# Optimization experiments

Hardware: AMD Instinct MI355X
Metric: run time of the kernel (lower is better)

## Reference

```python
import jax, jax.numpy as jnp
import numpy as np

H = 768
HEADS = 12
HD = H // HEADS
INTER = 3072
EPS = 1e-6


def setup_inputs() -> dict:
    key = jax.random.key(0)
    ks = jax.random.split(key, 10)
    B, T = 4, 1024
    scale = 0.02
    return {
        "x": jax.random.normal(ks[0], (B, T, H), jnp.float32),
        "mask": jnp.ones((B, T), jnp.float32),
        "w_qkv": jax.random.normal(ks[1], (H, 3 * H), jnp.float32) * scale,
        "w_o": jax.random.normal(ks[2], (H, H), jnp.float32) * scale,
        "tau": jnp.full((HEADS,), 5.0, jnp.float32),
        "w1": jax.random.normal(ks[3], (H, INTER), jnp.float32) * scale,
        "b1": jnp.zeros((INTER,), jnp.float32),
        "w2": jax.random.normal(ks[4], (INTER, H), jnp.float32) * scale,
        "b2": jnp.zeros((H,), jnp.float32),
        "nb1": jnp.zeros((H,), jnp.float32),
        "nb2": jnp.zeros((H,), jnp.float32),
    }


def _block(x, mask, w_qkv, w_o, tau, w1, b1, w2, b2, nb1, nb2):
    B, T, C = x.shape
    qkv = x @ w_qkv                                  # [B,T,3H]
    q, k, v = jnp.split(qkv, 3, axis=-1)
    q = q.reshape(B, T, HEADS, HD)
    k = k.reshape(B, T, HEADS, HD)
    v = v.reshape(B, T, HEADS, HD)
    # 2quad attention: quadratic-normalized scores instead of softmax
    s = jnp.einsum("bthd,bshd->bhts", q, k) / jnp.sqrt(jnp.float32(HD))
    s = s / tau[None, :, None, None]
    w = s * s                                        # [B,HEADS,T,T]
    w = w * mask[:, None, None, :]                   # zero masked keys
    w = w / (jnp.sum(w, axis=-1, keepdims=True) + EPS)
    out = jnp.einsum("bhts,bshd->bthd", w, v).reshape(B, T, C)
    out = out @ w_o
    x = x + 0.2 * out + nb1                          # scaled residual + bias-only norm1
    ffn = jax.nn.relu(x @ w1 + b1) @ w2 + b2
    x = x + ffn + nb2                                # residual + bias-only norm2
    return x


def reference(x, mask, w_qkv, w_o, tau, w1, b1, w2, b2, nb1, nb2):
    return _block(x, mask, w_qkv, w_o, tau, w1, b1, w2, b2, nb1, nb2)
```

## Files before the change

kernel.cpp:

```cpp
#include <hip/hip_runtime.h>

typedef __bf16 bf16x8 __attribute__((ext_vector_type(8)));
typedef float f32x4 __attribute__((ext_vector_type(4)));
typedef unsigned short u16;
typedef unsigned long long u64;

#define HDIM 768
#define NHEADS 12
#define SEQ 1024
#define NBATCH 4
#define ROWS 4096
#define QKV3 2304
#define INTERDIM 3072

__device__ __forceinline__ u16 f2bf(float f) {
  union { float f; unsigned int u; } v; v.f = f;
  unsigned int r = v.u + 0x7fffu + ((v.u >> 16) & 1u);
  return (u16)(r >> 16);
}

__device__ __forceinline__ float bf2f(u16 b) {
  union { unsigned int u; float f; } v; v.u = (unsigned int)b << 16;
  return v.f;
}

__device__ __forceinline__ void gload16(const u16* g, u16* l) {
  __builtin_amdgcn_global_load_lds(
      (const __attribute__((address_space(1))) void*)g,
      (__attribute__((address_space(3))) void*)l, 16, 0, 0);
}

__device__ __forceinline__ unsigned ldsoff(const void* p) {
  return (unsigned)(unsigned long long)(const __attribute__((address_space(3))) char*)p;
}

__device__ __forceinline__ u64 tr8(unsigned a) {
  u64 r;
  asm volatile("ds_read_b64_tr_b16 %0, %1" : "=v"(r) : "v"(a));
  return r;
}

union B8 { u64 q[2]; bf16x8 v; };

__global__ __launch_bounds__(256) void k_prep(
    const float* __restrict__ x, u16* __restrict__ xb,
    const float* __restrict__ wqkv, u16* __restrict__ wqkvT,
    const float* __restrict__ wo, u16* __restrict__ woT,
    const float* __restrict__ w1, u16* __restrict__ w1T,
    const float* __restrict__ w2, u16* __restrict__ w2T) {
  __shared__ float tile[32][33];
  int bid = blockIdx.x, tid = threadIdx.x;
  if (bid < 3072) {
    int i = bid * 256 + tid;
    float4 f = reinterpret_cast<const float4*>(x)[i];
    ushort4 o;
    o.x = f2bf(f.x); o.y = f2bf(f.y); o.z = f2bf(f.z); o.w = f2bf(f.w);
    reinterpret_cast<ushort4*>(xb)[i] = o;
    return;
  }
  const float* in; u16* outp; int K, N, t;
  if (bid < 4800)      { in = wqkv; outp = wqkvT; K = 768;  N = 2304; t = bid - 3072; }
  else if (bid < 5376) { in = wo;   outp = woT;   K = 768;  N = 768;  t = bid - 4800; }
  else if (bid < 7680) { in = w1;   outp = w1T;   K = 768;  N = 3072; t = bid - 5376; }
  else                 { in = w2;   outp = w2T;   K = 3072; N = 768;  t = bid - 7680; }
  int ntx = N >> 5;
  int bx = t % ntx, by = t / ntx;
  int tx = tid & 31, ty = tid >> 5;
  int n0 = bx * 32, k0 = by * 32;
#pragma unroll
  for (int i = 0; i < 32; i += 8)
    tile[ty + i][tx] = in[(size_t)(k0 + ty + i) * N + n0 + tx];
  __syncthreads();
#pragma unroll
  for (int i = 0; i < 32; i += 8)
    outp[(size_t)(n0 + ty + i) * K + k0 + tx] = f2bf(tile[tx][ty + i]);
}

template<int BM, int BN, int MODE>
__global__ __launch_bounds__(256, 2) void k_gemm(
    const u16* __restrict__ A, const u16* __restrict__ Bt,
    int M, int N, int K, int ksplit,
    u16* __restrict__ obf,
    const float* __restrict__ e1, const float* __restrict__ e2) {
  constexpr int BK = 32;
  constexpr int WC = (BN == 128) ? 2 : 1;
  constexpr int WR = 4 / WC;
  constexpr int WM = BM / WR;
  constexpr int WN = BN / WC;
  constexpr int MFR = WM / 16;
  constexpr int NFR = WN / 16;
  constexpr int AISS = BM / 64;
  constexpr int BISS = BN / 64;
  constexpr int ISS = AISS + BISS;
  __shared__ u16 As[2][BM * BK];
  __shared__ u16 Bs[2][BN * BK];
  int tid = threadIdx.x, lane = tid & 63, wid = tid >> 6;
  int wr = wid / WC, wc = wid % WC;
  int fr = lane & 15, fg = lane >> 4, fk = fg * 8;

  int gx = gridDim.x;
  int nwg = gx * gridDim.y;
  int orig = blockIdx.y * gx + blockIdx.x;
  int swz = (orig & 7) * (nwg >> 3) + (orig >> 3);
  int bx = swz % gx, by = swz / gx;
  int m0 = by * BM, n0 = bx * BN;
  int Kc = K / ksplit, k0 = blockIdx.z * Kc;

  f32x4 acc[MFR][NFR] = {};

  int r = tid >> 2;
  int cswz = ((tid & 3) * 8) ^ (((r >> 1) & 3) << 3);
  const u16* Ag = A + (size_t)(m0 + r) * K + k0 + cswz;
  const u16* Bg = Bt + (size_t)(n0 + r) * K + k0 + cswz;

#define STAGE(t2) do {                                                   \
    int b_ = (t2) & 1; int kt_ = (t2) * BK;                              \
    _Pragma("unroll")                                                    \
    for (int i_ = 0; i_ < AISS; i_++)                                    \
      gload16(Ag + kt_ + (size_t)(i_ * 64) * K, &As[b_][i_ * 2048 + wid * 512]); \
    _Pragma("unroll")                                                    \
    for (int i_ = 0; i_ < BISS; i_++)                                    \
      gload16(Bg + kt_ + (size_t)(i_ * 64) * K, &Bs[b_][i_ * 2048 + wid * 512]); \
  } while (0)

  int ce = fk ^ (((fr >> 1) & 3) << 3);

  int nt = Kc / BK;
  STAGE(0);
  STAGE(1);

  for (int t = 0; t < nt; t++) {
    int cur = t & 1;
    if (t == nt - 1) {
      asm volatile("s_waitcnt vmcnt(0)\n\ts_barrier" ::: "memory");
    } else if constexpr (ISS == 6) {
      asm volatile("s_waitcnt vmcnt(6)\n\ts_barrier" ::: "memory");
    } else if constexpr (ISS == 4) {
      asm volatile("s_waitcnt vmcnt(4)\n\ts_barrier" ::: "memory");
    } else {
      asm volatile("s_waitcnt vmcnt(3)\n\ts_barrier" ::: "memory");
    }

    bf16x8 af[MFR], bv[NFR];
#pragma unroll
    for (int mi = 0; mi < MFR; mi++)
      af[mi] = *reinterpret_cast<const bf16x8*>(&As[cur][(wr * WM + mi * 16 + fr) * BK + ce]);
#pragma unroll
    for (int ni = 0; ni < NFR; ni++)
      bv[ni] = *reinterpret_cast<const bf16x8*>(&Bs[cur][(wc * WN + ni * 16 + fr) * BK + ce]);

    asm volatile("s_waitcnt lgkmcnt(0)\n\ts_barrier" ::: "memory");
    if (t + 2 < nt) STAGE(t + 2);

    __builtin_amdgcn_s_setprio(1);
#pragma unroll
    for (int mi = 0; mi < MFR; mi++)
#pragma unroll
      for (int ni = 0; ni < NFR; ni++)
        acc[mi][ni] = __builtin_amdgcn_mfma_f32_16x16x32_bf16(af[mi], bv[ni], acc[mi][ni], 0, 0, 0);
    __builtin_amdgcn_s_setprio(0);
  }
#undef STAGE

  u16* outp = (MODE == 3) ? obf + (size_t)blockIdx.z * ((size_t)M * N) : obf;
#pragma unroll
  for (int mi = 0; mi < MFR; mi++) {
#pragma unroll
    for (int ni = 0; ni < NFR; ni++) {
#pragma unroll
      for (int i = 0; i < 4; i++) {
        int row = m0 + wr * WM + mi * 16 + fg * 4 + i;
        int col = n0 + wc * WN + ni * 16 + fr;
        float v = acc[mi][ni][i];
        size_t idx = (size_t)row * N + col;
        if constexpr (MODE == 0) {
          outp[idx] = f2bf(v);
        } else if constexpr (MODE == 1) {
          outp[idx] = f2bf(e1[idx] + 0.2f * v + e2[col]);
        } else if constexpr (MODE == 2) {
          float t = v + e1[col];
          outp[idx] = f2bf(t > 0.f ? t : 0.f);
        } else {
          outp[idx] = f2bf(v);
        }
      }
    }
  }
}

__global__ void k_ffn2_reduce(const u16* __restrict__ p, const u16* __restrict__ x1b,
                              const float* __restrict__ b2, const float* __restrict__ nb2,
                              float* __restrict__ out) {
  int i = blockIdx.x * 256 + threadIdx.x;
  int col4 = (i * 4) % HDIM;
  ushort4 xv = reinterpret_cast<const ushort4*>(x1b)[i];
  float4 bb = *reinterpret_cast<const float4*>(b2 + col4);
  float4 nn = *reinterpret_cast<const float4*>(nb2 + col4);
  float4 s;
  s.x = bf2f(xv.x) + bb.x + nn.x;
  s.y = bf2f(xv.y) + bb.y + nn.y;
  s.z = bf2f(xv.z) + bb.z + nn.z;
  s.w = bf2f(xv.w) + bb.w + nn.w;
#pragma unroll
  for (int z = 0; z < 4; z++) {
    ushort4 pv = reinterpret_cast<const ushort4*>(p + (size_t)z * ROWS * HDIM)[i];
    s.x += bf2f(pv.x); s.y += bf2f(pv.y); s.z += bf2f(pv.z); s.w += bf2f(pv.w);
  }
  reinterpret_cast<float4*>(out)[i] = s;
}

__global__ __launch_bounds__(512) void k_attn(
    const u16* __restrict__ qkv, const float* __restrict__ mask,
    const float* __restrict__ tau, u16* __restrict__ outp) {
  __shared__ u16 Ks[64 * 72];
  __shared__ u16 Vs[64 * 64];
  __shared__ u16 Ps[8 * 1024];
  int tid = threadIdx.x, lane = tid & 63, w = tid >> 6;
  int bid = blockIdx.x;
  int bh = bid % 48, t0i = bid / 48;
  int h = bh >> 2, b = bh & 3;
  int fr = lane & 15, fg = lane >> 4, fk = fg * 8;
  int rb = b * SEQ;
  float rs = 1.0f / (8.0f * tau[h]);
  float rs2 = rs * rs;

  int t0 = t0i * 128 + w * 16;
  const u16* qrow = qkv + (size_t)(rb + t0 + fr) * QKV3 + h * 64;
  bf16x8 aq0 = *reinterpret_cast<const bf16x8*>(qrow + fk);
  bf16x8 aq1 = *reinterpret_cast<const bf16x8*>(qrow + 32 + fk);

  f32x4 acco[4] = {};
  f32x4 accd = {};

  int sr = tid >> 3, c = tid & 7;
  const u16* kg = qkv + (size_t)(rb + sr) * QKV3 + HDIM + h * 64 + c * 8;
  const u16* vg = kg + HDIM;
  u16* kw = &Ks[sr * 72 + c * 8];
  u16* vw = &Vs[((sr >> 2) * 4 + (c >> 1)) * 64 + (sr & 3) * 16 + (c & 1) * 8];
  unsigned psb = ldsoff(&Ps[w * 1024]);
  unsigned vsb = ldsoff(Vs);

  __bf16 onev = (__bf16)1.0f;
  bf16x8 ones = {onev, onev, onev, onev, onev, onev, onev, onev};

  int4 kreg = *reinterpret_cast<const int4*>(kg);
  int4 vreg = *reinterpret_cast<const int4*>(vg);

  for (int st = 0; st < SEQ; st += 64) {
    __syncthreads();
    *reinterpret_cast<int4*>(kw) = kreg;
    *reinterpret_cast<int4*>(vw) = vreg;
    __syncthreads();
    if (st + 64 < SEQ) {
      kreg = *reinterpret_cast<const int4*>(kg + (size_t)(st + 64) * QKV3);
      vreg = *reinterpret_cast<const int4*>(vg + (size_t)(st + 64) * QKV3);
    }

#pragma unroll
    for (int sf = 0; sf < 4; sf++) {
      bf16x8 bk0 = *reinterpret_cast<const bf16x8*>(&Ks[(sf * 16 + fr) * 72 + fk]);
      bf16x8 bk1 = *reinterpret_cast<const bf16x8*>(&Ks[(sf * 16 + fr) * 72 + 32 + fk]);
      f32x4 s = {};
      s = __builtin_amdgcn_mfma_f32_16x16x32_bf16(aq0, bk0, s, 0, 0, 0);
      s = __builtin_amdgcn_mfma_f32_16x16x32_bf16(aq1, bk1, s, 0, 0, 0);
      float rm = rs2 * mask[b * SEQ + st + sf * 16 + fr];
      u64 pw = 0;
#pragma unroll
      for (int i = 0; i < 4; i++) {
        float wv = s[i] * s[i] * rm;
        pw |= (u64)f2bf(wv) << (16 * i);
      }
      *reinterpret_cast<u64*>(&Ps[w * 1024 + (sf * 4 + (fr >> 2)) * 64 + (fr & 3) * 16 + fg * 4]) = pw;
    }
    asm volatile("s_waitcnt lgkmcnt(0)" ::: "memory");
    __builtin_amdgcn_sched_barrier(0);

    u64 pa0 = tr8(psb + (fg * 2 + 0) * 128 + fr * 2);
    u64 pa1 = tr8(psb + (fg * 2 + 1) * 128 + fr * 2);
    u64 pa2 = tr8(psb + (8 + fg * 2 + 0) * 128 + fr * 2);
    u64 pa3 = tr8(psb + (8 + fg * 2 + 1) * 128 + fr * 2);
    u64 vb[4][4];
#pragma unroll
    for (int df = 0; df < 4; df++) {
      vb[df][0] = tr8(vsb + ((fg * 2 + 0) * 4 + df) * 128 + fr * 2);
      vb[df][1] = tr8(vsb + ((fg * 2 + 1) * 4 + df) * 128 + fr * 2);
      vb[df][2] = tr8(vsb + ((8 + fg * 2 + 0) * 4 + df) * 128 + fr * 2);
      vb[df][3] = tr8(vsb + ((8 + fg * 2 + 1) * 4 + df) * 128 + fr * 2);
    }
    asm volatile("s_waitcnt lgkmcnt(0)" ::: "memory");
    __builtin_amdgcn_sched_barrier(0);

    B8 ap0, ap1;
    ap0.q[0] = pa0; ap0.q[1] = pa1;
    ap1.q[0] = pa2; ap1.q[1] = pa3;
#pragma unroll
    for (int df = 0; df < 4; df++) {
      B8 b0, b1;
      b0.q[0] = vb[df][0]; b0.q[1] = vb[df][1];
      b1.q[0] = vb[df][2]; b1.q[1] = vb[df][3];
      acco[df] = __builtin_amdgcn_mfma_f32_16x16x32_bf16(ap0.v, b0.v, acco[df], 0, 0, 0);
      acco[df] = __builtin_amdgcn_mfma_f32_16x16x32_bf16(ap1.v, b1.v, acco[df], 0, 0, 0);
    }
    accd = __builtin_amdgcn_mfma_f32_16x16x32_bf16(ap0.v, ones, accd, 0, 0, 0);
    accd = __builtin_amdgcn_mfma_f32_16x16x32_bf16(ap1.v, ones, accd, 0, 0, 0);
  }

#pragma unroll
  for (int df = 0; df < 4; df++)
#pragma unroll
    for (int i = 0; i < 4; i++) {
      int t = t0 + fg * 4 + i;
      int col = h * 64 + df * 16 + fr;
      float o = acco[df][i] / (accd[i] + 1e-6f);
      outp[(size_t)(rb + t) * HDIM + col] = f2bf(o);
    }
}

extern "C" void kernel_launch(void* const* d_in, const int* in_sizes, int n_in,
                              void* d_out, int out_size, void* d_ws, size_t ws_size,
                              hipStream_t stream) {
  const float* x     = (const float*)d_in[0];
  const float* mask  = (const float*)d_in[1];
  const float* w_qkv = (const float*)d_in[2];
  const float* w_o   = (const float*)d_in[3];
  const float* tau   = (const float*)d_in[4];
  const float* w1    = (const float*)d_in[5];
  const float* b1    = (const float*)d_in[6];
  const float* w2    = (const float*)d_in[7];
  const float* b2    = (const float*)d_in[8];
  const float* nb1   = (const float*)d_in[9];
  const float* nb2   = (const float*)d_in[10];
  float* out = (float*)d_out;
  (void)ws_size; (void)in_sizes; (void)n_in; (void)out_size;

  char* base = (char*)d_ws;
  u16* partb = (u16*)base;
  u16* xb    = (u16*)(base);
  u16* wqkvT = (u16*)(base + 6291456);
  u16* woT   = (u16*)(base + 9830400);
  u16* w1T   = (u16*)(base + 11010048);
  u16* qkvb  = (u16*)(base + 15728640);
  u16* attnb = (u16*)(base + 34603008);
  u16* x1b   = (u16*)(base + 40894464);
  u16* w2T   = (u16*)(base + 50331648);
  u16* hb    = (u16*)(base + 67633152);

  k_prep<<<9984, 256, 0, stream>>>(x, xb, w_qkv, wqkvT, w_o, woT, w1, w1T, w2, w2T);

  k_gemm<256, 128, 0><<<dim3(QKV3 / 128, ROWS / 256), 256, 0, stream>>>(
      xb, wqkvT, ROWS, QKV3, HDIM, 1, qkvb, nullptr, nullptr);
  k_attn<<<384, 512, 0, stream>>>(qkvb, mask, tau, attnb);
  k_gemm<128, 64, 1><<<dim3(HDIM / 64, ROWS / 128), 256, 0, stream>>>(
      attnb, woT, ROWS, HDIM, HDIM, 1, x1b, x, nb1);
  k_gemm<128, 128, 2><<<dim3(INTERDIM / 128, ROWS / 128), 256, 0, stream>>>(
      x1b, w1T, ROWS, INTERDIM, HDIM, 1, hb, b1, nullptr);
  k_gemm<128, 128, 3><<<dim3(HDIM / 128, ROWS / 128, 4), 256, 0, stream>>>(
      hb, w2T, ROWS, HDIM, INTERDIM, 4, partb, nullptr, nullptr);
  k_ffn2_reduce<<<ROWS * HDIM / 4 / 256, 256, 0, stream>>>(partb, x1b, b2, nb2, out);
}
```

Measured before the change: 150.1 us.

## Restructure attention: smaller blocks, K in registers, double-buffered V in LDS

The attention kernel moves from 512-thread blocks covering 128 query rows to 256-thread blocks covering 64 rows, which doubles the grid to 768 blocks. K fragments are now loaded straight from global memory into registers per wave, so the K shared-memory tile goes away. V is double-buffered in LDS so there is one barrier per iteration instead of two. The aim is more blocks in flight and less synchronisation overhead. The cost is that each wave loads K redundantly from global memory and register pressure rises.

```diff
diff --git a/kernel.cpp b/kernel.cpp
--- a/kernel.cpp
+++ b/kernel.cpp
@@ -209,12 +209,11 @@
   reinterpret_cast<float4*>(out)[i] = s;
 }
 
-__global__ __launch_bounds__(512) void k_attn(
+__global__ __launch_bounds__(256) void k_attn(
     const u16* __restrict__ qkv, const float* __restrict__ mask,
     const float* __restrict__ tau, u16* __restrict__ outp) {
-  __shared__ u16 Ks[64 * 72];
-  __shared__ u16 Vs[64 * 64];
-  __shared__ u16 Ps[8 * 1024];
+  __shared__ u16 Vs[2][64 * 64];
+  __shared__ u16 Ps[4][1024];
   int tid = threadIdx.x, lane = tid & 63, w = tid >> 6;
   int bid = blockIdx.x;
   int bh = bid % 48, t0i = bid / 48;
@@ -224,45 +223,53 @@
   float rs = 1.0f / (8.0f * tau[h]);
   float rs2 = rs * rs;
 
-  int t0 = t0i * 128 + w * 16;
+  int t0 = t0i * 64 + w * 16;
   const u16* qrow = qkv + (size_t)(rb + t0 + fr) * QKV3 + h * 64;
   bf16x8 aq0 = *reinterpret_cast<const bf16x8*>(qrow + fk);
   bf16x8 aq1 = *reinterpret_cast<const bf16x8*>(qrow + 32 + fk);
 
+  const u16* kb = qkv + (size_t)rb * QKV3 + HDIM + h * 64;
+
   f32x4 acco[4] = {};
   f32x4 accd = {};
 
-  int sr = tid >> 3, c = tid & 7;
-  const u16* kg = qkv + (size_t)(rb + sr) * QKV3 + HDIM + h * 64 + c * 8;
-  const u16* vg = kg + HDIM;
-  u16* kw = &Ks[sr * 72 + c * 8];
-  u16* vw = &Vs[((sr >> 2) * 4 + (c >> 1)) * 64 + (sr & 3) * 16 + (c & 1) * 8];
-  unsigned psb = ldsoff(&Ps[w * 1024]);
-  unsigned vsb = ldsoff(Vs);
+  int sr = tid >> 2, c2 = tid & 3;
+  const u16* vg = qkv + (size_t)(rb + sr) * QKV3 + 2 * HDIM + h * 64 + c2 * 16;
+  int vwo = ((sr >> 2) * 4 + c2) * 64 + (sr & 3) * 16;
+  unsigned psb = ldsoff(&Ps[w][0]);
+  unsigned vsb0 = ldsoff(&Vs[0][0]);
 
   __bf16 onev = (__bf16)1.0f;
   bf16x8 ones = {onev, onev, onev, onev, onev, onev, onev, onev};
 
-  int4 kreg = *reinterpret_cast<const int4*>(kg);
-  int4 vreg = *reinterpret_cast<const int4*>(vg);
-
-  for (int st = 0; st < SEQ; st += 64) {
-    __syncthreads();
-    *reinterpret_cast<int4*>(kw) = kreg;
-    *reinterpret_cast<int4*>(vw) = vreg;
-    __syncthreads();
-    if (st + 64 < SEQ) {
-      kreg = *reinterpret_cast<const int4*>(kg + (size_t)(st + 64) * QKV3);
-      vreg = *reinterpret_cast<const int4*>(vg + (size_t)(st + 64) * QKV3);
+  int4 v0 = *reinterpret_cast<const int4*>(vg);
+  int4 v1 = *reinterpret_cast<const int4*>(vg + 8);
+  *reinterpret_cast<int4*>(&Vs[0][vwo]) = v0;
+  *reinterpret_cast<int4*>(&Vs[0][vwo + 8]) = v1;
+  bf16x8 bk[4][2];
+#pragma unroll
+  for (int sf = 0; sf < 4; sf++) {
+    const u16* kr = kb + (size_t)(sf * 16 + fr) * QKV3;
+    bk[sf][0] = *reinterpret_cast<const bf16x8*>(kr + fk);
+    bk[sf][1] = *reinterpret_cast<const bf16x8*>(kr + 32 + fk);
+  }
+  __syncthreads();
+
+  for (int t = 0; t < 16; t++) {
+    int st = t * 64;
+    unsigned vsb = vsb0 + (t & 1) * 8192;
+    bool pf = (t < 15);
+
+    if (pf) {
+      v0 = *reinterpret_cast<const int4*>(vg + (size_t)(st + 64) * QKV3);
+      v1 = *reinterpret_cast<const int4*>(vg + (size_t)(st + 64) * QKV3 + 8);
     }
 
 #pragma unroll
     for (int sf = 0; sf < 4; sf++) {
-      bf16x8 bk0 = *reinterpret_cast<const bf16x8*>(&Ks[(sf * 16 + fr) * 72 + fk]);
-      bf16x8 bk1 = *reinterpret_cast<const bf16x8*>(&Ks[(sf * 16 + fr) * 72 + 32 + fk]);
       f32x4 s = {};
-      s = __builtin_amdgcn_mfma_f32_16x16x32_bf16(aq0, bk0, s, 0, 0, 0);
-      s = __builtin_amdgcn_mfma_f32_16x16x32_bf16(aq1, bk1, s, 0, 0, 0);
+      s = __builtin_amdgcn_mfma_f32_16x16x32_bf16(aq0, bk[sf][0], s, 0, 0, 0);
+      s = __builtin_amdgcn_mfma_f32_16x16x32_bf16(aq1, bk[sf][1], s, 0, 0, 0);
       float rm = rs2 * mask[b * SEQ + st + sf * 16 + fr];
       u64 pw = 0;
 #pragma unroll
@@ -270,8 +277,18 @@
         float wv = s[i] * s[i] * rm;
         pw |= (u64)f2bf(wv) << (16 * i);
       }
-      *reinterpret_cast<u64*>(&Ps[w * 1024 + (sf * 4 + (fr >> 2)) * 64 + (fr & 3) * 16 + fg * 4]) = pw;
-    }
+      *reinterpret_cast<u64*>(&Ps[w][(sf * 4 + (fr >> 2)) * 64 + (fr & 3) * 16 + fg * 4]) = pw;
+    }
+
+    if (pf) {
+#pragma unroll
+      for (int sf = 0; sf < 4; sf++) {
+        const u16* kr = kb + (size_t)(st + 64 + sf * 16 + fr) * QKV3;
+        bk[sf][0] = *reinterpret_cast<const bf16x8*>(kr + fk);
+        bk[sf][1] = *reinterpret_cast<const bf16x8*>(kr + 32 + fk);
+      }
+    }
+
     asm volatile("s_waitcnt lgkmcnt(0)" ::: "memory");
     __builtin_amdgcn_sched_barrier(0);
 
@@ -303,6 +320,13 @@
     }
     accd = __builtin_amdgcn_mfma_f32_16x16x32_bf16(ap0.v, ones, accd, 0, 0, 0);
     accd = __builtin_amdgcn_mfma_f32_16x16x32_bf16(ap1.v, ones, accd, 0, 0, 0);
+
+    if (pf) {
+      u16* vdst = &Vs[(t + 1) & 1][vwo];
+      *reinterpret_cast<int4*>(vdst) = v0;
+      *reinterpret_cast<int4*>(vdst + 8) = v1;
+    }
+    __syncthreads();
   }
 
 #pragma unroll
@@ -349,7 +373,7 @@
 
   k_gemm<256, 128, 0><<<dim3(QKV3 / 128, ROWS / 256), 256, 0, stream>>>(
       xb, wqkvT, ROWS, QKV3, HDIM, 1, qkvb, nullptr, nullptr);
-  k_attn<<<384, 512, 0, stream>>>(qkvb, mask, tau, attnb);
+  k_attn<<<768, 256, 0, stream>>>(qkvb, mask, tau, attnb);
   k_gemm<128, 64, 1><<<dim3(HDIM / 64, ROWS / 128), 256, 0, stream>>>(
       attnb, woT, ROWS, HDIM, HDIM, 1, x1b, x, nb1);
   k_gemm<128, 128, 2><<<dim3(INTERDIM / 128, ROWS / 128), 256, 0, stream>>>(
```

Result: slower. 168.7 us (+12.4%).
